# Optimization experiments

Hardware: AMD Instinct MI355X
Metric: run time of the kernel (lower is better)

The kernel has to match this reference:

```python
import jax, jax.numpy as jnp
import numpy as np

HEADS = 4
DIM_HEAD = 64
SCALE = DIM_HEAD ** -0.5


def setup_inputs() -> dict:
    key = jax.random.key(0)
    k1, k2, k3 = jax.random.split(key, 3)
    C = 256
    hidden = HEADS * DIM_HEAD  # 256
    x = jax.random.normal(k1, (16, C, 64, 64), dtype=jnp.float32)
    # 1x1 conv weights collapsed to [out, in] matrices
    w_qkv = jax.random.normal(k2, (3 * hidden, C), dtype=jnp.float32) * (C ** -0.5)
    w_out = jax.random.normal(k3, (C, hidden), dtype=jnp.float32) * (hidden ** -0.5)
    b_out = jnp.zeros((C,), dtype=jnp.float32)
    return {"x": x, "w_qkv": w_qkv, "w_out": w_out, "b_out": b_out}


def reference(x, w_qkv, w_out, b_out):
    b, c, h, w = x.shape
    n = h * w
    # 1x1 conv == channel GEMM
    qkv = jnp.einsum('bchw,oc->bohw', x, w_qkv)           # [b, 3*hidden, h, w]
    qkv = qkv.reshape(b, 3, HEADS, DIM_HEAD, n)            # [b, 3, H, d, n]
    q, k, v = qkv[:, 0], qkv[:, 1], qkv[:, 2]              # each [b, H, d, n]
    q = jax.nn.softmax(q, axis=2) * SCALE                  # softmax over d
    k = jax.nn.softmax(k, axis=3)                          # softmax over n
    context = jnp.einsum('bhdn,bhen->bhde', k, v)          # [b, H, d, e]
    out = jnp.einsum('bhde,bhdn->bhen', context, q)        # [b, H, e, n]
    out = out.reshape(b, HEADS * DIM_HEAD, h, w)           # [b, hidden, h, w]
    return jnp.einsum('bchw,oc->bohw', out, w_out) + b_out[None, :, None, None]
```

## Files before the change

kernel.cpp:

```cpp
#include <hip/hip_runtime.h>

#define NPIX 4096
#define SCALE 0.125f

typedef _Float16 half8 __attribute__((ext_vector_type(8)));
typedef _Float16 half4 __attribute__((ext_vector_type(4)));
typedef float floatx4 __attribute__((ext_vector_type(4)));

__device__ __forceinline__ void async16(void* lds, const void* g) {
  __builtin_amdgcn_global_load_lds(
      (const __attribute__((address_space(1))) unsigned int*)(uintptr_t)g,
      (__attribute__((address_space(3))) unsigned int*)(unsigned)(uintptr_t)lds,
      16, 0, 0);
}

__global__ __launch_bounds__(256) void split16_kernel(const float* __restrict__ w,
                                                      _Float16* __restrict__ hi,
                                                      _Float16* __restrict__ lo, int n) {
  int i = blockIdx.x * 256 + threadIdx.x;
  if (i < n) {
    float v = w[i];
    _Float16 h = (_Float16)v;
    hi[i] = h;
    lo[i] = (_Float16)(v - (float)h);
  }
}

__global__ __launch_bounds__(256) void transpose16_kernel(const float* __restrict__ x,
                                                          _Float16* __restrict__ xt) {
  __shared__ float t[64][65];
  const int n0 = blockIdx.x * 64, c0 = blockIdx.y * 64, b = blockIdx.z;
  const float* xp = x + (long)b * 256 * NPIX;
  const int tid = threadIdx.x;
  const int r = tid >> 4, c4 = (tid & 15) * 4;
#pragma unroll
  for (int p = 0; p < 4; p++) {
    float4 v = *(const float4*)&xp[(long)(c0 + r + p * 16) * NPIX + n0 + c4];
    t[r + p * 16][c4 + 0] = v.x;
    t[r + p * 16][c4 + 1] = v.y;
    t[r + p * 16][c4 + 2] = v.z;
    t[r + p * 16][c4 + 3] = v.w;
  }
  __syncthreads();
  const int n = tid >> 2, cg = (tid & 3) * 16;
  alignas(16) _Float16 o[16];
#pragma unroll
  for (int i = 0; i < 16; i++) o[i] = (_Float16)t[cg + i][n];
  _Float16* dst = &xt[((long)b * NPIX + n0 + n) * 256 + c0 + cg];
  *(float4*)dst = *(float4*)&o[0];
  *(float4*)(dst + 8) = *(float4*)&o[8];
}

__global__ __launch_bounds__(256) void q_gemm_softmax(const _Float16* __restrict__ Ahp,
                                                      const _Float16* __restrict__ Alp,
                                                      const _Float16* __restrict__ Bt,
                                                      _Float16* __restrict__ PT) {
  union alignas(16) QU {
    _Float16 st[2][3][128 * 32];
    _Float16 pt[128][128];
  };
  __shared__ QU u;
  const int tid = threadIdx.x;
  const int n0 = blockIdx.x * 128, m0 = blockIdx.y * 128;
  const int bz = blockIdx.z;
  const _Float16* Bp = Bt + (long)bz * NPIX * 256;
  const int wv = tid >> 6, l = tid & 63;
  const int r16 = l & 15, q = l >> 4;
  const int mb = (wv >> 1) * 64, nb = (wv & 1) * 64;
  const int r1 = tid >> 2;
  const int o1 = ((tid & 3) * 8) ^ (((r1 >> 1) & 3) * 8);
  const int r2 = r1 + 64;
  const int ldsc1 = (wv * 64) * 8;
  const int ldsc2 = (256 + wv * 64) * 8;
  const int q8 = (q * 8) ^ (((r16 >> 1) & 3) * 8);

  auto STAGE = [&](int buf, int kt) {
    const int k0 = kt * 32;
    async16(&u.st[buf][0][ldsc1], &Ahp[(long)(m0 + r1) * 256 + k0 + o1]);
    async16(&u.st[buf][0][ldsc2], &Ahp[(long)(m0 + r2) * 256 + k0 + o1]);
    async16(&u.st[buf][1][ldsc1], &Alp[(long)(m0 + r1) * 256 + k0 + o1]);
    async16(&u.st[buf][1][ldsc2], &Alp[(long)(m0 + r2) * 256 + k0 + o1]);
    async16(&u.st[buf][2][ldsc1], &Bp[(long)(n0 + r1) * 256 + k0 + o1]);
    async16(&u.st[buf][2][ldsc2], &Bp[(long)(n0 + r2) * 256 + k0 + o1]);
  };

  floatx4 acc[4][4];
#pragma unroll
  for (int i = 0; i < 4; i++)
#pragma unroll
    for (int j = 0; j < 4; j++) acc[i][j] = (floatx4){0.f, 0.f, 0.f, 0.f};

  STAGE(0, 0);
  __syncthreads();
  int cur = 0;
  for (int kt = 0; kt < 8; kt++) {
    if (kt < 7) STAGE(cur ^ 1, kt + 1);
    half8 fa[4], flo[4], fb[4];
#pragma unroll
    for (int i = 0; i < 4; i++) {
      fa[i] = *(const half8*)&u.st[cur][0][(mb + i * 16 + r16) * 32 + q8];
      flo[i] = *(const half8*)&u.st[cur][1][(mb + i * 16 + r16) * 32 + q8];
      fb[i] = *(const half8*)&u.st[cur][2][(nb + i * 16 + r16) * 32 + q8];
    }
#pragma unroll
    for (int i = 0; i < 4; i++)
#pragma unroll
      for (int j = 0; j < 4; j++) {
        acc[i][j] = __builtin_amdgcn_mfma_f32_16x16x32_f16(fa[i], fb[j], acc[i][j], 0, 0, 0);
        acc[i][j] = __builtin_amdgcn_mfma_f32_16x16x32_f16(flo[i], fb[j], acc[i][j], 0, 0, 0);
      }
    __syncthreads();
    cur ^= 1;
  }

#pragma unroll
  for (int j = 0; j < 4; j++) {
    float s = 0.f;
#pragma unroll
    for (int i = 0; i < 4; i++)
#pragma unroll
      for (int t = 0; t < 4; t++) {
        float e = __expf(acc[i][j][t]);
        acc[i][j][t] = e;
        s += e;
      }
    s += __shfl_xor(s, 16, 64);
    s += __shfl_xor(s, 32, 64);
    const float rinv = 1.0f / s;
    const int nl = nb + j * 16 + r16;
    const int swz = (nl & 7) * 8;
#pragma unroll
    for (int i = 0; i < 4; i++) {
      half4 h4;
#pragma unroll
      for (int t = 0; t < 4; t++) h4[t] = (_Float16)(acc[i][j][t] * rinv);
      *(half4*)&u.pt[nl][(mb + i * 16 + q * 4) ^ swz] = h4;
    }
  }
  __syncthreads();
  const int rbase = tid >> 4, c16 = tid & 15;
  _Float16* dst = PT + ((long)(bz * 2 + (m0 >> 7)) * NPIX + n0) * 128;
#pragma unroll
  for (int k = 0; k < 8; k++) {
    const int row = rbase + k * 16;
    const int chunk = c16 ^ (row & 7);
    float4 v = *(const float4*)&u.pt[row][chunk * 8];
    *(float4*)&dst[(long)row * 128 + c16 * 8] = v;
  }
}

#define CPB 4
__global__ __launch_bounds__(256) void kv_ctx_gemm(const _Float16* __restrict__ Ahp,
                                                   const _Float16* __restrict__ Alp,
                                                   const _Float16* __restrict__ Bt,
                                                   float* __restrict__ pbuf,
                                                   float* __restrict__ rsbuf) {
  union alignas(16) KVU {
    _Float16 st[2][3][128 * 32];
    _Float16 ev[128][136];
  };
  __shared__ KVU u;
  const int tid = threadIdx.x;
  const int cg = blockIdx.x;
  const int hi = blockIdx.y;
  const int b = blockIdx.z;
  const _Float16* Bp = Bt + (long)b * NPIX * 256;
  const int wv = tid >> 6, l = tid & 63;
  const int r16 = l & 15, q = l >> 4;
  const int mb = (wv >> 1) * 64, nb = (wv & 1) * 64;
  const int r1 = tid >> 2;
  const int o1 = ((tid & 3) * 8) ^ (((r1 >> 1) & 3) * 8);
  const int ldsc1 = (wv * 64) * 8;
  const int ldsc2 = (256 + wv * 64) * 8;
  const int q8 = (q * 8) ^ (((r16 >> 1) & 3) * 8);
  const long gAk = (long)(256 + hi * 64 + r1) * 256;
  const long gAv = (long)(512 + hi * 64 + r1) * 256;

  auto STAGE = [&](int buf, int kt, int n0) {
    const int k0 = kt * 32;
    async16(&u.st[buf][0][ldsc1], &Ahp[gAk + k0 + o1]);
    async16(&u.st[buf][0][ldsc2], &Ahp[gAv + k0 + o1]);
    async16(&u.st[buf][1][ldsc1], &Alp[gAk + k0 + o1]);
    async16(&u.st[buf][1][ldsc2], &Alp[gAv + k0 + o1]);
    async16(&u.st[buf][2][ldsc1], &Bp[(long)(n0 + r1) * 256 + k0 + o1]);
    async16(&u.st[buf][2][ldsc2], &Bp[(long)(n0 + 64 + r1) * 256 + k0 + o1]);
  };

  floatx4 c2[4];
#pragma unroll
  for (int j = 0; j < 4; j++) c2[j] = (floatx4){0.f, 0.f, 0.f, 0.f};
  float rs = 0.f;

  for (int cs = 0; cs < CPB; cs++) {
    const int n0 = (cg * CPB + cs) * 128;
    floatx4 acc[4][4];
#pragma unroll
    for (int i = 0; i < 4; i++)
#pragma unroll
      for (int j = 0; j < 4; j++) acc[i][j] = (floatx4){0.f, 0.f, 0.f, 0.f};

    STAGE(0, 0, n0);
    __syncthreads();
    int cur = 0;
    for (int kt = 0; kt < 8; kt++) {
      if (kt < 7) STAGE(cur ^ 1, kt + 1, n0);
      half8 fa[4], flo[4], fb[4];
#pragma unroll
      for (int i = 0; i < 4; i++) {
        fa[i] = *(const half8*)&u.st[cur][0][(mb + i * 16 + r16) * 32 + q8];
        flo[i] = *(const half8*)&u.st[cur][1][(mb + i * 16 + r16) * 32 + q8];
        fb[i] = *(const half8*)&u.st[cur][2][(nb + i * 16 + r16) * 32 + q8];
      }
#pragma unroll
      for (int i = 0; i < 4; i++)
#pragma unroll
        for (int j = 0; j < 4; j++) {
          acc[i][j] = __builtin_amdgcn_mfma_f32_16x16x32_f16(fa[i], fb[j], acc[i][j], 0, 0, 0);
          acc[i][j] = __builtin_amdgcn_mfma_f32_16x16x32_f16(flo[i], fb[j], acc[i][j], 0, 0, 0);
        }
      __syncthreads();
      cur ^= 1;
    }

    const bool is_k = (mb == 0);
#pragma unroll
    for (int i = 0; i < 4; i++) {
      const int row = mb + i * 16 + q * 4;
#pragma unroll
      for (int j = 0; j < 4; j++) {
        const int col = nb + j * 16 + r16;
#pragma unroll
        for (int t = 0; t < 4; t++) {
          const float vv0 = acc[i][j][t];
          u.ev[row + t][col] = (_Float16)(is_k ? __expf(vv0) : vv0);
        }
      }
    }
    __syncthreads();

#pragma unroll
    for (int ks = 0; ks < 4; ks++) {
      half8 a = *(const half8*)&u.ev[wv * 16 + r16][ks * 32 + q * 8];
#pragma unroll
      for (int ii = 0; ii < 8; ii++) rs += (float)a[ii];
#pragma unroll
      for (int j = 0; j < 4; j++) {
        half8 bv = *(const half8*)&u.ev[64 + j * 16 + r16][ks * 32 + q * 8];
        c2[j] = __builtin_amdgcn_mfma_f32_16x16x32_f16(a, bv, c2[j], 0, 0, 0);
      }
    }
    __syncthreads();
  }

  rs += __shfl_xor(rs, 16, 64);
  rs += __shfl_xor(rs, 32, 64);
  const int bh = b * 4 + hi;
  float* pp = pbuf + ((long)bh * 8 + cg) * 4096;
#pragma unroll
  for (int j = 0; j < 4; j++)
#pragma unroll
    for (int reg = 0; reg < 4; reg++)
      pp[(wv * 16 + q * 4 + reg) * 64 + j * 16 + r16] = c2[j][reg];
  if (l < 16) rsbuf[((long)bh * 8 + cg) * 64 + wv * 16 + r16] = rs;
}

__global__ __launch_bounds__(256) void reduce_ctx(const float* __restrict__ pbuf,
                                                  float* __restrict__ ctx) {
  int g = blockIdx.x * 256 + threadIdx.x;
  int bh = g >> 12, e = g & 4095;
  const float* pp = pbuf + ((long)bh * 8) * 4096 + e;
  float s = 0.f;
#pragma unroll
  for (int c = 0; c < 8; c++) s += pp[(long)c * 4096];
  ctx[g] = s;
}

__global__ __launch_bounds__(256) void zinv_kernel(const float* __restrict__ rsbuf,
                                                   float* __restrict__ kinvz) {
  int g = blockIdx.x * 256 + threadIdx.x;
  int bh = g >> 6, d = g & 63;
  const float* rp = rsbuf + (long)bh * 8 * 64 + d;
  float s = 0.f;
#pragma unroll
  for (int c = 0; c < 8; c++) s += rp[c * 64];
  kinvz[g] = 1.0f / s;
}

__global__ __launch_bounds__(256) void mctx_kernel(const float* __restrict__ w_out,
                                                   const float* __restrict__ ctx,
                                                   const float* __restrict__ kinvz,
                                                   _Float16* __restrict__ Mhi,
                                                   _Float16* __restrict__ Mlo) {
  __shared__ float sctxT[64][65];
  const int cq = blockIdx.x, h = blockIdx.y, b = blockIdx.z;
  const int bh = b * 4 + h;
  const float* cp = ctx + (long)bh * 4096;
  const int tid = threadIdx.x;
  {
    const int d = tid >> 2, e0 = (tid & 3) * 16;
#pragma unroll
    for (int k = 0; k < 4; k++) {
      float4 v = *(const float4*)&cp[d * 64 + e0 + k * 4];
      sctxT[e0 + k * 4 + 0][d] = v.x;
      sctxT[e0 + k * 4 + 1][d] = v.y;
      sctxT[e0 + k * 4 + 2][d] = v.z;
      sctxT[e0 + k * 4 + 3][d] = v.w;
    }
  }
  __syncthreads();
  const int c = cq * 64 + (tid >> 2);
  const int d0 = (tid & 3) * 16;
  const float* wp = w_out + (long)c * 256 + h * 64;
  float acc[16];
#pragma unroll
  for (int i = 0; i < 16; i++) acc[i] = 0.f;
#pragma unroll
  for (int e4 = 0; e4 < 16; e4++) {
    float4 wv = *(const float4*)&wp[e4 * 4];
#pragma unroll
    for (int u2 = 0; u2 < 4; u2++) {
      const float we = ((const float*)&wv)[u2];
      const int e = e4 * 4 + u2;
#pragma unroll
      for (int dd = 0; dd < 16; dd++) acc[dd] = fmaf(we, sctxT[e][d0 + dd], acc[dd]);
    }
  }
  alignas(16) _Float16 hi16[16], lo16[16];
#pragma unroll
  for (int k4 = 0; k4 < 4; k4++) {
    float4 zv = *(const float4*)&kinvz[bh * 64 + d0 + k4 * 4];
#pragma unroll
    for (int u2 = 0; u2 < 4; u2++) {
      const int dd = k4 * 4 + u2;
      float v = acc[dd] * (SCALE * ((const float*)&zv)[u2]);
      _Float16 hh = (_Float16)v;
      hi16[dd] = hh;
      lo16[dd] = (_Float16)(v - (float)hh);
    }
  }
  _Float16* mh = Mhi + ((long)b * 256 + c) * 256 + h * 64 + d0;
  _Float16* ml = Mlo + ((long)b * 256 + c) * 256 + h * 64 + d0;
#pragma unroll
  for (int k = 0; k < 2; k++) {
    *(float4*)&mh[k * 8] = *(float4*)&hi16[k * 8];
    *(float4*)&ml[k * 8] = *(float4*)&lo16[k * 8];
  }
}

__global__ __launch_bounds__(256) void out_gemm(const _Float16* __restrict__ Mhi,
                                                const _Float16* __restrict__ Mlo,
                                                const _Float16* __restrict__ PT,
                                                float* __restrict__ C,
                                                const float* __restrict__ bias) {
  __shared__ _Float16 st[2][3][128 * 32];
  const int tid = threadIdx.x;
  const int n0 = blockIdx.x * 128, m0 = blockIdx.y * 128;
  const int b = blockIdx.z;
  const _Float16* Ah = Mhi + (long)b * 65536;
  const _Float16* Al = Mlo + (long)b * 65536;
  float* Cp = C + (long)b * 256 * NPIX;
  const int wv = tid >> 6, l = tid & 63;
  const int r16 = l & 15, q = l >> 4;
  const int mb = (wv >> 1) * 64, nb = (wv & 1) * 64;
  const int r1 = tid >> 2;
  const int o1 = ((tid & 3) * 8) ^ (((r1 >> 1) & 3) * 8);
  const int r2 = r1 + 64;
  const int ldsc1 = (wv * 64) * 8;
  const int ldsc2 = (256 + wv * 64) * 8;
  const int q8 = (q * 8) ^ (((r16 >> 1) & 3) * 8);

  auto STAGE = [&](int buf, int kt) {
    const int k0 = kt * 32;
    async16(&st[buf][0][ldsc1], &Ah[(long)(m0 + r1) * 256 + k0 + o1]);
    async16(&st[buf][0][ldsc2], &Ah[(long)(m0 + r2) * 256 + k0 + o1]);
    async16(&st[buf][1][ldsc1], &Al[(long)(m0 + r1) * 256 + k0 + o1]);
    async16(&st[buf][1][ldsc2], &Al[(long)(m0 + r2) * 256 + k0 + o1]);
    const _Float16* Bk = PT + ((long)(b * 2 + (kt >> 2)) * NPIX + n0) * 128;
    async16(&st[buf][2][ldsc1], &Bk[(long)r1 * 128 + (kt & 3) * 32 + o1]);
    async16(&st[buf][2][ldsc2], &Bk[(long)(r1 + 64) * 128 + (kt & 3) * 32 + o1]);
  };

  floatx4 acc[4][4];
#pragma unroll
  for (int i = 0; i < 4; i++)
#pragma unroll
    for (int j = 0; j < 4; j++) acc[i][j] = (floatx4){0.f, 0.f, 0.f, 0.f};

  STAGE(0, 0);
  __syncthreads();
  int cur = 0;
  for (int kt = 0; kt < 8; kt++) {
    if (kt < 7) STAGE(cur ^ 1, kt + 1);
    half8 fa[4], flo[4], fb[4];
#pragma unroll
    for (int i = 0; i < 4; i++) {
      fa[i] = *(const half8*)&st[cur][0][(mb + i * 16 + r16) * 32 + q8];
      flo[i] = *(const half8*)&st[cur][1][(mb + i * 16 + r16) * 32 + q8];
      fb[i] = *(const half8*)&st[cur][2][(nb + i * 16 + r16) * 32 + q8];
    }
#pragma unroll
    for (int i = 0; i < 4; i++)
#pragma unroll
      for (int j = 0; j < 4; j++) {
        acc[i][j] = __builtin_amdgcn_mfma_f32_16x16x32_f16(fa[i], fb[j], acc[i][j], 0, 0, 0);
        acc[i][j] = __builtin_amdgcn_mfma_f32_16x16x32_f16(flo[i], fb[j], acc[i][j], 0, 0, 0);
      }
    __syncthreads();
    cur ^= 1;
  }
#pragma unroll
  for (int i = 0; i < 4; i++) {
    const int mrow = m0 + mb + i * 16 + q * 4;
#pragma unroll
    for (int t = 0; t < 4; t++) {
      float bz = bias[mrow + t];
#pragma unroll
      for (int j = 0; j < 4; j++) {
        Cp[(long)(mrow + t) * NPIX + n0 + nb + j * 16 + r16] = acc[i][j][t] + bz;
      }
    }
  }
}

extern "C" void kernel_launch(void* const* d_in, const int* in_sizes, int n_in,
                              void* d_out, int out_size, void* d_ws, size_t ws_size,
                              hipStream_t stream) {
  const float* x = (const float*)d_in[0];
  const float* w_qkv = (const float*)d_in[1];
  const float* w_out = (const float*)d_in[2];
  const float* b_out = (const float*)d_in[3];
  float* out = (float*)d_out;

  _Float16* PT = (_Float16*)d_ws;
  float* ctx = (float*)(PT + (long)16 * 2 * NPIX * 128);
  float* kinvz = ctx + 64 * 4096;
  float* rsbuf = kinvz + 4096;
  _Float16* wq_hi = (_Float16*)(rsbuf + 64 * 8 * 64);
  _Float16* wq_lo = wq_hi + 768 * 256;
  _Float16* Mhi = wq_lo + 768 * 256;
  _Float16* Mlo = Mhi + 16 * 256 * 256;
  _Float16* xt = (_Float16*)d_out;
  float* pbuf = (float*)d_out + (1 << 23);

  split16_kernel<<<768, 256, 0, stream>>>(w_qkv, wq_hi, wq_lo, 768 * 256);
  transpose16_kernel<<<dim3(64, 4, 16), 256, 0, stream>>>(x, xt);
  kv_ctx_gemm<<<dim3(8, 4, 16), 256, 0, stream>>>(wq_hi, wq_lo, xt, pbuf, rsbuf);
  reduce_ctx<<<1024, 256, 0, stream>>>(pbuf, ctx);
  zinv_kernel<<<16, 256, 0, stream>>>(rsbuf, kinvz);
  q_gemm_softmax<<<dim3(32, 2, 16), 256, 0, stream>>>(wq_hi, wq_lo, xt, PT);
  mctx_kernel<<<dim3(4, 4, 16), 256, 0, stream>>>(w_out, ctx, kinvz, Mhi, Mlo);
  out_gemm<<<dim3(32, 2, 16), 256, 0, stream>>>(Mhi, Mlo, PT, out, b_out);
}
```

Baseline: 214.6 us.

## Widen GEMM tiles to 128x256 with 512-thread blocks across three kernels

Each of q_gemm_softmax, kv_ctx_gemm and out_gemm now uses 512-thread blocks of 8 waves, each block covering 256 columns instead of 128. The A-operand hi/lo tiles are staged once and shared by twice as many columns, which cuts redundant global and LDS traffic for the weight operand. Grids shrink to match, and kv_ctx_gemm now writes 16 partials per head instead of 8, so reduce_ctx and zinv sum over 16. The cost is more LDS per block, fewer blocks in flight, and extra reduction traffic.

```diff
diff --git a/kernel.cpp b/kernel.cpp
--- a/kernel.cpp
+++ b/kernel.cpp
@@ -51,37 +51,35 @@
   *(float4*)(dst + 8) = *(float4*)&o[8];
 }
 
-__global__ __launch_bounds__(256) void q_gemm_softmax(const _Float16* __restrict__ Ahp,
-                                                      const _Float16* __restrict__ Alp,
-                                                      const _Float16* __restrict__ Bt,
-                                                      _Float16* __restrict__ PT) {
+
+__global__ __launch_bounds__(512, 4) void q_gemm_softmax(const _Float16* __restrict__ Ahp,
+                                                         const _Float16* __restrict__ Alp,
+                                                         const _Float16* __restrict__ Bt,
+                                                         _Float16* __restrict__ PT) {
   union alignas(16) QU {
-    _Float16 st[2][3][128 * 32];
-    _Float16 pt[128][128];
+    _Float16 st[2][16384];
+    _Float16 pt[256][128];
   };
   __shared__ QU u;
   const int tid = threadIdx.x;
-  const int n0 = blockIdx.x * 128, m0 = blockIdx.y * 128;
+  const int n0 = blockIdx.x * 256, m0 = blockIdx.y * 128;
   const int bz = blockIdx.z;
   const _Float16* Bp = Bt + (long)bz * NPIX * 256;
   const int wv = tid >> 6, l = tid & 63;
   const int r16 = l & 15, q = l >> 4;
-  const int mb = (wv >> 1) * 64, nb = (wv & 1) * 64;
+  const int mb = (wv >> 2) * 64, nb = (wv & 3) * 64;
   const int r1 = tid >> 2;
   const int o1 = ((tid & 3) * 8) ^ (((r1 >> 1) & 3) * 8);
-  const int r2 = r1 + 64;
-  const int ldsc1 = (wv * 64) * 8;
-  const int ldsc2 = (256 + wv * 64) * 8;
+  const int ldsA = wv * 512;
   const int q8 = (q * 8) ^ (((r16 >> 1) & 3) * 8);
 
   auto STAGE = [&](int buf, int kt) {
     const int k0 = kt * 32;
-    async16(&u.st[buf][0][ldsc1], &Ahp[(long)(m0 + r1) * 256 + k0 + o1]);
-    async16(&u.st[buf][0][ldsc2], &Ahp[(long)(m0 + r2) * 256 + k0 + o1]);
-    async16(&u.st[buf][1][ldsc1], &Alp[(long)(m0 + r1) * 256 + k0 + o1]);
-    async16(&u.st[buf][1][ldsc2], &Alp[(long)(m0 + r2) * 256 + k0 + o1]);
-    async16(&u.st[buf][2][ldsc1], &Bp[(long)(n0 + r1) * 256 + k0 + o1]);
-    async16(&u.st[buf][2][ldsc2], &Bp[(long)(n0 + r2) * 256 + k0 + o1]);
+    _Float16* base = u.st[buf];
+    async16(&base[ldsA], &Ahp[(long)(m0 + r1) * 256 + k0 + o1]);
+    async16(&base[4096 + ldsA], &Alp[(long)(m0 + r1) * 256 + k0 + o1]);
+    async16(&base[8192 + ldsA], &Bp[(long)(n0 + r1) * 256 + k0 + o1]);
+    async16(&base[12288 + ldsA], &Bp[(long)(n0 + 128 + r1) * 256 + k0 + o1]);
   };
 
   floatx4 acc[4][4];
@@ -98,9 +96,9 @@
     half8 fa[4], flo[4], fb[4];
 #pragma unroll
     for (int i = 0; i < 4; i++) {
-      fa[i] = *(const half8*)&u.st[cur][0][(mb + i * 16 + r16) * 32 + q8];
-      flo[i] = *(const half8*)&u.st[cur][1][(mb + i * 16 + r16) * 32 + q8];
-      fb[i] = *(const half8*)&u.st[cur][2][(nb + i * 16 + r16) * 32 + q8];
+      fa[i] = *(const half8*)&u.st[cur][(mb + i * 16 + r16) * 32 + q8];
+      flo[i] = *(const half8*)&u.st[cur][4096 + (mb + i * 16 + r16) * 32 + q8];
+      fb[i] = *(const half8*)&u.st[cur][8192 + (nb + i * 16 + r16) * 32 + q8];
     }
 #pragma unroll
     for (int i = 0; i < 4; i++)
@@ -142,22 +140,22 @@
   _Float16* dst = PT + ((long)(bz * 2 + (m0 >> 7)) * NPIX + n0) * 128;
 #pragma unroll
   for (int k = 0; k < 8; k++) {
-    const int row = rbase + k * 16;
+    const int row = rbase + k * 32;
     const int chunk = c16 ^ (row & 7);
     float4 v = *(const float4*)&u.pt[row][chunk * 8];
     *(float4*)&dst[(long)row * 128 + c16 * 8] = v;
   }
 }
 
-#define CPB 4
-__global__ __launch_bounds__(256) void kv_ctx_gemm(const _Float16* __restrict__ Ahp,
-                                                   const _Float16* __restrict__ Alp,
-                                                   const _Float16* __restrict__ Bt,
-                                                   float* __restrict__ pbuf,
-                                                   float* __restrict__ rsbuf) {
+#define CPB 2
+__global__ __launch_bounds__(512, 4) void kv_ctx_gemm(const _Float16* __restrict__ Ahp,
+                                                      const _Float16* __restrict__ Alp,
+                                                      const _Float16* __restrict__ Bt,
+                                                      float* __restrict__ pbuf,
+                                                      float* __restrict__ rsbuf) {
   union alignas(16) KVU {
-    _Float16 st[2][3][128 * 32];
-    _Float16 ev[128][136];
+    _Float16 st[2][16384];
+    _Float16 ev[128][264];
   };
   __shared__ KVU u;
   const int tid = threadIdx.x;
@@ -167,32 +165,30 @@
   const _Float16* Bp = Bt + (long)b * NPIX * 256;
   const int wv = tid >> 6, l = tid & 63;
   const int r16 = l & 15, q = l >> 4;
-  const int mb = (wv >> 1) * 64, nb = (wv & 1) * 64;
+  const int mb = (wv >> 2) * 64, nb = (wv & 3) * 64;
   const int r1 = tid >> 2;
   const int o1 = ((tid & 3) * 8) ^ (((r1 >> 1) & 3) * 8);
-  const int ldsc1 = (wv * 64) * 8;
-  const int ldsc2 = (256 + wv * 64) * 8;
+  const int ldsA = wv * 512;
   const int q8 = (q * 8) ^ (((r16 >> 1) & 3) * 8);
-  const long gAk = (long)(256 + hi * 64 + r1) * 256;
-  const long gAv = (long)(512 + hi * 64 + r1) * 256;
+  const long gA = (long)((r1 < 64 ? 256 : 448) + hi * 64 + r1) * 256;
 
   auto STAGE = [&](int buf, int kt, int n0) {
     const int k0 = kt * 32;
-    async16(&u.st[buf][0][ldsc1], &Ahp[gAk + k0 + o1]);
-    async16(&u.st[buf][0][ldsc2], &Ahp[gAv + k0 + o1]);
-    async16(&u.st[buf][1][ldsc1], &Alp[gAk + k0 + o1]);
-    async16(&u.st[buf][1][ldsc2], &Alp[gAv + k0 + o1]);
-    async16(&u.st[buf][2][ldsc1], &Bp[(long)(n0 + r1) * 256 + k0 + o1]);
-    async16(&u.st[buf][2][ldsc2], &Bp[(long)(n0 + 64 + r1) * 256 + k0 + o1]);
+    _Float16* base = u.st[buf];
+    async16(&base[ldsA], &Ahp[gA + k0 + o1]);
+    async16(&base[4096 + ldsA], &Alp[gA + k0 + o1]);
+    async16(&base[8192 + ldsA], &Bp[(long)(n0 + r1) * 256 + k0 + o1]);
+    async16(&base[12288 + ldsA], &Bp[(long)(n0 + 128 + r1) * 256 + k0 + o1]);
   };
 
   floatx4 c2[4];
 #pragma unroll
   for (int j = 0; j < 4; j++) c2[j] = (floatx4){0.f, 0.f, 0.f, 0.f};
   float rs = 0.f;
+  const int h2 = wv >> 2, dblk = wv & 3;
 
   for (int cs = 0; cs < CPB; cs++) {
-    const int n0 = (cg * CPB + cs) * 128;
+    const int n0 = (cg * CPB + cs) * 256;
     floatx4 acc[4][4];
 #pragma unroll
     for (int i = 0; i < 4; i++)
@@ -207,9 +203,9 @@
       half8 fa[4], flo[4], fb[4];
 #pragma unroll
       for (int i = 0; i < 4; i++) {
-        fa[i] = *(const half8*)&u.st[cur][0][(mb + i * 16 + r16) * 32 + q8];
-        flo[i] = *(const half8*)&u.st[cur][1][(mb + i * 16 + r16) * 32 + q8];
-        fb[i] = *(const half8*)&u.st[cur][2][(nb + i * 16 + r16) * 32 + q8];
+        fa[i] = *(const half8*)&u.st[cur][(mb + i * 16 + r16) * 32 + q8];
+        flo[i] = *(const half8*)&u.st[cur][4096 + (mb + i * 16 + r16) * 32 + q8];
+        fb[i] = *(const half8*)&u.st[cur][8192 + (nb + i * 16 + r16) * 32 + q8];
       }
 #pragma unroll
       for (int i = 0; i < 4; i++)
@@ -240,12 +236,12 @@
 
 #pragma unroll
     for (int ks = 0; ks < 4; ks++) {
-      half8 a = *(const half8*)&u.ev[wv * 16 + r16][ks * 32 + q * 8];
+      half8 a = *(const half8*)&u.ev[dblk * 16 + r16][h2 * 128 + ks * 32 + q * 8];
 #pragma unroll
       for (int ii = 0; ii < 8; ii++) rs += (float)a[ii];
 #pragma unroll
       for (int j = 0; j < 4; j++) {
-        half8 bv = *(const half8*)&u.ev[64 + j * 16 + r16][ks * 32 + q * 8];
+        half8 bv = *(const half8*)&u.ev[64 + j * 16 + r16][h2 * 128 + ks * 32 + q * 8];
         c2[j] = __builtin_amdgcn_mfma_f32_16x16x32_f16(a, bv, c2[j], 0, 0, 0);
       }
     }
@@ -255,23 +251,24 @@
   rs += __shfl_xor(rs, 16, 64);
   rs += __shfl_xor(rs, 32, 64);
   const int bh = b * 4 + hi;
-  float* pp = pbuf + ((long)bh * 8 + cg) * 4096;
+  const int part = cg * 2 + h2;
+  float* pp = pbuf + ((long)bh * 16 + part) * 4096;
 #pragma unroll
   for (int j = 0; j < 4; j++)
 #pragma unroll
     for (int reg = 0; reg < 4; reg++)
-      pp[(wv * 16 + q * 4 + reg) * 64 + j * 16 + r16] = c2[j][reg];
-  if (l < 16) rsbuf[((long)bh * 8 + cg) * 64 + wv * 16 + r16] = rs;
+      pp[(dblk * 16 + q * 4 + reg) * 64 + j * 16 + r16] = c2[j][reg];
+  if (l < 16) rsbuf[((long)bh * 16 + part) * 64 + dblk * 16 + r16] = rs;
 }
 
 __global__ __launch_bounds__(256) void reduce_ctx(const float* __restrict__ pbuf,
                                                   float* __restrict__ ctx) {
   int g = blockIdx.x * 256 + threadIdx.x;
   int bh = g >> 12, e = g & 4095;
-  const float* pp = pbuf + ((long)bh * 8) * 4096 + e;
+  const float* pp = pbuf + ((long)bh * 16) * 4096 + e;
   float s = 0.f;
 #pragma unroll
-  for (int c = 0; c < 8; c++) s += pp[(long)c * 4096];
+  for (int c = 0; c < 16; c++) s += pp[(long)c * 4096];
   ctx[g] = s;
 }
 
@@ -279,10 +276,10 @@
                                                    float* __restrict__ kinvz) {
   int g = blockIdx.x * 256 + threadIdx.x;
   int bh = g >> 6, d = g & 63;
-  const float* rp = rsbuf + (long)bh * 8 * 64 + d;
+  const float* rp = rsbuf + (long)bh * 16 * 64 + d;
   float s = 0.f;
 #pragma unroll
-  for (int c = 0; c < 8; c++) s += rp[c * 64];
+  for (int c = 0; c < 16; c++) s += rp[c * 64];
   kinvz[g] = 1.0f / s;
 }
 
@@ -347,37 +344,34 @@
   }
 }
 
-__global__ __launch_bounds__(256) void out_gemm(const _Float16* __restrict__ Mhi,
-                                                const _Float16* __restrict__ Mlo,
-                                                const _Float16* __restrict__ PT,
-                                                float* __restrict__ C,
-                                                const float* __restrict__ bias) {
-  __shared__ _Float16 st[2][3][128 * 32];
+__global__ __launch_bounds__(512, 4) void out_gemm(const _Float16* __restrict__ Mhi,
+                                                   const _Float16* __restrict__ Mlo,
+                                                   const _Float16* __restrict__ PT,
+                                                   float* __restrict__ C,
+                                                   const float* __restrict__ bias) {
+  __shared__ _Float16 st[2][16384];
   const int tid = threadIdx.x;
-  const int n0 = blockIdx.x * 128, m0 = blockIdx.y * 128;
+  const int n0 = blockIdx.x * 256, m0 = blockIdx.y * 128;
   const int b = blockIdx.z;
   const _Float16* Ah = Mhi + (long)b * 65536;
   const _Float16* Al = Mlo + (long)b * 65536;
   float* Cp = C + (long)b * 256 * NPIX;
   const int wv = tid >> 6, l = tid & 63;
   const int r16 = l & 15, q = l >> 4;
-  const int mb = (wv >> 1) * 64, nb = (wv & 1) * 64;
+  const int mb = (wv >> 2) * 64, nb = (wv & 3) * 64;
   const int r1 = tid >> 2;
   const int o1 = ((tid & 3) * 8) ^ (((r1 >> 1) & 3) * 8);
-  const int r2 = r1 + 64;
-  const int ldsc1 = (wv * 64) * 8;
-  const int ldsc2 = (256 + wv * 64) * 8;
+  const int ldsA = wv * 512;
   const int q8 = (q * 8) ^ (((r16 >> 1) & 3) * 8);
 
   auto STAGE = [&](int buf, int kt) {
     const int k0 = kt * 32;
-    async16(&st[buf][0][ldsc1], &Ah[(long)(m0 + r1) * 256 + k0 + o1]);
-    async16(&st[buf][0][ldsc2], &Ah[(long)(m0 + r2) * 256 + k0 + o1]);
-    async16(&st[buf][1][ldsc1], &Al[(long)(m0 + r1) * 256 + k0 + o1]);
-    async16(&st[buf][1][ldsc2], &Al[(long)(m0 + r2) * 256 + k0 + o1]);
+    _Float16* base = st[buf];
+    async16(&base[ldsA], &Ah[(long)(m0 + r1) * 256 + k0 + o1]);
+    async16(&base[4096 + ldsA], &Al[(long)(m0 + r1) * 256 + k0 + o1]);
     const _Float16* Bk = PT + ((long)(b * 2 + (kt >> 2)) * NPIX + n0) * 128;
-    async16(&st[buf][2][ldsc1], &Bk[(long)r1 * 128 + (kt & 3) * 32 + o1]);
-    async16(&st[buf][2][ldsc2], &Bk[(long)(r1 + 64) * 128 + (kt & 3) * 32 + o1]);
+    async16(&base[8192 + ldsA], &Bk[(long)r1 * 128 + (kt & 3) * 32 + o1]);
+    async16(&base[12288 + ldsA], &Bk[(long)(r1 + 128) * 128 + (kt & 3) * 32 + o1]);
   };
 
   floatx4 acc[4][4];
@@ -394,9 +388,9 @@
     half8 fa[4], flo[4], fb[4];
 #pragma unroll
     for (int i = 0; i < 4; i++) {
-      fa[i] = *(const half8*)&st[cur][0][(mb + i * 16 + r16) * 32 + q8];
-      flo[i] = *(const half8*)&st[cur][1][(mb + i * 16 + r16) * 32 + q8];
-      fb[i] = *(const half8*)&st[cur][2][(nb + i * 16 + r16) * 32 + q8];
+      fa[i] = *(const half8*)&st[cur][(mb + i * 16 + r16) * 32 + q8];
+      flo[i] = *(const half8*)&st[cur][4096 + (mb + i * 16 + r16) * 32 + q8];
+      fb[i] = *(const half8*)&st[cur][8192 + (nb + i * 16 + r16) * 32 + q8];
     }
 #pragma unroll
     for (int i = 0; i < 4; i++)
@@ -435,7 +429,7 @@
   float* ctx = (float*)(PT + (long)16 * 2 * NPIX * 128);
   float* kinvz = ctx + 64 * 4096;
   float* rsbuf = kinvz + 4096;
-  _Float16* wq_hi = (_Float16*)(rsbuf + 64 * 8 * 64);
+  _Float16* wq_hi = (_Float16*)(rsbuf + 64 * 16 * 64);
   _Float16* wq_lo = wq_hi + 768 * 256;
   _Float16* Mhi = wq_lo + 768 * 256;
   _Float16* Mlo = Mhi + 16 * 256 * 256;
@@ -444,10 +438,10 @@
 
   split16_kernel<<<768, 256, 0, stream>>>(w_qkv, wq_hi, wq_lo, 768 * 256);
   transpose16_kernel<<<dim3(64, 4, 16), 256, 0, stream>>>(x, xt);
-  kv_ctx_gemm<<<dim3(8, 4, 16), 256, 0, stream>>>(wq_hi, wq_lo, xt, pbuf, rsbuf);
+  kv_ctx_gemm<<<dim3(8, 4, 16), 512, 0, stream>>>(wq_hi, wq_lo, xt, pbuf, rsbuf);
   reduce_ctx<<<1024, 256, 0, stream>>>(pbuf, ctx);
   zinv_kernel<<<16, 256, 0, stream>>>(rsbuf, kinvz);
-  q_gemm_softmax<<<dim3(32, 2, 16), 256, 0, stream>>>(wq_hi, wq_lo, xt, PT);
+  q_gemm_softmax<<<dim3(16, 2, 16), 512, 0, stream>>>(wq_hi, wq_lo, xt, PT);
   mctx_kernel<<<dim3(4, 4, 16), 256, 0, stream>>>(w_out, ctx, kinvz, Mhi, Mlo);
-  out_gemm<<<dim3(32, 2, 16), 256, 0, stream>>>(Mhi, Mlo, PT, out, b_out);
-}
+  out_gemm<<<dim3(16, 2, 16), 512, 0, stream>>>(Mhi, Mlo, PT, out, b_out);
+}
```

New measurement: 254.5 us. +18.6%, slower.
